# Optimization experiments

Measured on AMD Instinct MI355X. Metric: run time of the kernel, lower is better.

The kernel has to match this reference:

```python
import jax, jax.numpy as jnp
import numpy as np

H = 1024      # hidden_size
L = 4         # num_layers
DI = 2 * H    # d_inner (expand=2)
N = 16        # d_state
K = 4         # d_conv
BATCH = 2
S = 1024
EPS = 1e-5


def _layernorm(x, g, b):
    mu = jnp.mean(x, axis=-1, keepdims=True)
    xc = x - mu
    var = jnp.mean(xc * xc, axis=-1, keepdims=True)
    return xc * jax.lax.rsqrt(var + EPS) * g + b


def _causal_dwconv(x, w, b):
    # x: [B,S,DI], w: [DI,K], b: [DI]. Torch Conv1d(pad=K-1, groups=DI) truncated to S == causal left-pad conv.
    xp = jnp.pad(x, ((0, 0), (K - 1, 0), (0, 0)))
    s = x.shape[1]
    y = sum(xp[:, k:k + s, :] * w[:, k] for k in range(K))
    return y + b


def _forward(hidden_states, in_norm_g, in_norm_b, ln_g, ln_b, in_proj_w,
             conv_w, conv_b, x_proj_w, dt_proj_w, dt_proj_b, D,
             mamba_ln_g, mamba_ln_b, out_proj_w, op1_w, op1_b, op2_w, op2_b):
    dtype = hidden_states.dtype
    A = -jnp.arange(1, N + 1, dtype=dtype)  # [N]; == -exp(log(arange)), identical across d_inner rows
    x = _layernorm(hidden_states, in_norm_g, in_norm_b)
    for l in range(L):
        res_x = x
        xn = _layernorm(x, ln_g[l], ln_b[l])
        xr = jnp.einsum('bsh,ph->bsp', xn, in_proj_w[l])           # [B,S,2*DI]
        x_inner, res = jnp.split(xr, 2, axis=-1)
        x_inner = jax.nn.silu(x_inner)
        for c in range(2):
            x_inner = jax.nn.silu(_causal_dwconv(x_inner, conv_w[l, c], conv_b[l, c]))
        proj = jnp.einsum('bsd,pd->bsp', x_inner, x_proj_w[l])     # [B,S,1+2N]
        dt_raw, Bm, Cm = proj[..., :1], proj[..., 1:1 + N], proj[..., 1 + N:]
        dt = jax.nn.softplus(dt_raw * dt_proj_w[l][:, 0] + dt_proj_b[l])  # [B,S,DI]

        def step(h, inp_t):
            dt_t, x_t, B_t, C_t = inp_t                      # [B,DI],[B,DI],[B,N],[B,N]
            h = h + dt_t[..., None] * (h * A + x_t[..., None] * B_t[:, None, :])
            y = jnp.einsum('bdn,bn->bd', h, C_t)
            return h, y

        h0 = jnp.zeros((x.shape[0], DI, N), dtype=dtype)
        xs = (dt.transpose(1, 0, 2), x_inner.transpose(1, 0, 2),
              Bm.transpose(1, 0, 2), Cm.transpose(1, 0, 2))
        _, ys = jax.lax.scan(step, h0, xs)                   # ys: [S,B,DI]
        y = ys.transpose(1, 0, 2)
        y = y + x_inner * D[l]
        y = _layernorm(y, mamba_ln_g[l], mamba_ln_b[l])
        y = y * jax.nn.sigmoid(res)
        x = res_x + jnp.einsum('bsd,hd->bsh', y, out_proj_w[l])
    out = jax.nn.gelu(x @ op1_w.T + op1_b, approximate=False) @ op2_w.T + op2_b
    return out + hidden_states


def setup_inputs() -> dict:
    key = jax.random.key(0)
    ks = jax.random.split(key, 10)
    rn = lambda k, shape, s: jax.random.normal(k, shape, dtype=jnp.float32) * s
    return {
        'hidden_states': rn(ks[0], (BATCH, S, H), 1.0),
        'in_norm_g': jnp.ones((H,), jnp.float32),
        'in_norm_b': jnp.zeros((H,), jnp.float32),
        'ln_g': jnp.ones((L, H), jnp.float32),
        'ln_b': jnp.zeros((L, H), jnp.float32),
        'in_proj_w': rn(ks[1], (L, 2 * DI, H), 0.02),
        'conv_w': rn(ks[2], (L, 2, DI, K), 0.2),
        'conv_b': jnp.zeros((L, 2, DI), jnp.float32),
        'x_proj_w': rn(ks[3], (L, 1 + 2 * N, DI), 0.02),
        'dt_proj_w': rn(ks[4], (L, DI, 1), 0.01),
        'dt_proj_b': jnp.full((L, DI), -4.0, jnp.float32),  # keeps dt small -> stable scan
        'D': jnp.ones((L, DI), jnp.float32),
        'mamba_ln_g': jnp.ones((L, DI), jnp.float32),
        'mamba_ln_b': jnp.zeros((L, DI), jnp.float32),
        'out_proj_w': rn(ks[5], (L, H, DI), 0.02),
        'op1_w': rn(ks[6], (H, H), 0.02),
        'op1_b': jnp.zeros((H,), jnp.float32),
        'op2_w': rn(ks[7], (H, H), 0.02),
        'op2_b': jnp.zeros((H,), jnp.float32),
    }


def reference(hidden_states, in_norm_g, in_norm_b, ln_g, ln_b, in_proj_w,
              conv_w, conv_b, x_proj_w, dt_proj_w, dt_proj_b, D,
              mamba_ln_g, mamba_ln_b, out_proj_w, op1_w, op1_b, op2_w, op2_b):
    return _forward(hidden_states, in_norm_g, in_norm_b, ln_g, ln_b, in_proj_w,
                    conv_w, conv_b, x_proj_w, dt_proj_w, dt_proj_b, D,
                    mamba_ln_g, mamba_ln_b, out_proj_w, op1_w, op1_b, op2_w, op2_b)
```

## Files before the change

kernel.cpp:

```cpp
#include <hip/hip_runtime.h>
#include <hip/hip_bf16.h>
#include <math.h>

constexpr int HDIM = 1024;
constexpr int LNUM = 4;
constexpr int DINNER = 2048;
constexpr int KCONV = 4;
constexpr int NB = 2;
constexpr int SLEN = 1024;
constexpr int TOK = NB * SLEN;
constexpr float LNEPS = 1e-5f;

constexpr int NCHUNK = 32;
constexpr int CLEN = SLEN / NCHUNK;
constexpr int PROW = 36;
constexpr int XPN = 48;
constexpr int XSPLIT = 8;

typedef __attribute__((ext_vector_type(8))) short short8;
typedef __attribute__((ext_vector_type(4))) float f32x4;

__device__ __forceinline__ float bf2f(__hip_bfloat16 x) { return __bfloat162float(x); }
__device__ __forceinline__ __hip_bfloat16 f2bf(float x) { return __float2bfloat16(x); }
__device__ __forceinline__ float sigmoidf_(float x) { return 1.f / (1.f + __expf(-x)); }
__device__ __forceinline__ float siluf_(float x) { return x / (1.f + __expf(-x)); }
__device__ __forceinline__ float softplusf_(float x) { return (x > 20.f) ? x : log1pf(__expf(x)); }

__device__ __forceinline__ float ldin(const void* p, size_t i, int f) {
    return f ? ((const float*)p)[i] : bf2f(((const __hip_bfloat16*)p)[i]);
}

__device__ __forceinline__ void cp16(const void* g, void* l) {
    __builtin_amdgcn_global_load_lds(
        (const __attribute__((address_space(1))) unsigned int*)g,
        (__attribute__((address_space(3))) unsigned int*)l, 16, 0, 0);
}

__global__ void probe_k(const unsigned* __restrict__ dtb, int* __restrict__ flag)
{
    if (threadIdx.x == 0 && blockIdx.x == 0)
        *flag = (dtb[0] == 0xC0800000u) ? 1 : 0;
}

__global__ __launch_bounds__(256) void cvt_k(const void* __restrict__ in, size_t off,
                                             __hip_bfloat16* __restrict__ out, int n,
                                             const int* __restrict__ dflag)
{
    const int f = *dflag;
    int i = blockIdx.x * 256 + threadIdx.x;
    if (i < n) out[i] = f2bf(ldin(in, off + (size_t)i, f));
}

template<int MODE, int D>
__global__ __launch_bounds__(256) void ln_k(
    const void* __restrict__ in, const void* __restrict__ g, const void* __restrict__ b,
    size_t goff,
    float* __restrict__ outF, __hip_bfloat16* __restrict__ outB,
    const float* __restrict__ gate, int gstride, const int* __restrict__ dflag)
{
    const int f = *dflag;
    constexpr int EPT = D / 256;
    const int t = blockIdx.x, tid = threadIdx.x;
    float v[EPT];
    float s1 = 0.f, s2 = 0.f;
#pragma unroll
    for (int i = 0; i < EPT; ++i) {
        int idx = tid + i * 256;
        float val = (MODE == 0) ? ldin(in, (size_t)t * D + idx, f)
                                : ((const float*)in)[(size_t)t * D + idx];
        v[i] = val; s1 += val; s2 += val * val;
    }
#pragma unroll
    for (int off = 32; off; off >>= 1) { s1 += __shfl_down(s1, off); s2 += __shfl_down(s2, off); }
    __shared__ float rs[4], rq[4];
    const int w = tid >> 6, lane = tid & 63;
    if (lane == 0) { rs[w] = s1; rq[w] = s2; }
    __syncthreads();
    const float mu = (rs[0] + rs[1] + rs[2] + rs[3]) * (1.f / D);
    const float ms = (rq[0] + rq[1] + rq[2] + rq[3]) * (1.f / D);
    const float var = ms - mu * mu;
    const float rstd = rsqrtf((var > 0.f ? var : 0.f) + LNEPS);
#pragma unroll
    for (int i = 0; i < EPT; ++i) {
        int idx = tid + i * 256;
        float o = (v[i] - mu) * rstd * ldin(g, goff + idx, f) + ldin(b, goff + idx, f);
        if (MODE == 2) o *= sigmoidf_(gate[(size_t)t * gstride + idx]);
        if (MODE == 0) outF[(size_t)t * D + idx] = o;
        else           outB[(size_t)t * D + idx] = f2bf(o);
    }
}

template<int EPI>
__global__ __launch_bounds__(256) void gemm_bt(
    const unsigned short* __restrict__ A, const unsigned short* __restrict__ B,
    int M, int N, int Kd,
    float* __restrict__ Cf, __hip_bfloat16* __restrict__ Cb,
    const float* __restrict__ resF, const void* __restrict__ bias,
    const void* __restrict__ resB, void* __restrict__ outD,
    const int* __restrict__ dflag)
{
    const int f = (EPI >= 2) ? *dflag : 0;
    __shared__ __align__(16) unsigned short As[2][128 * 32];
    __shared__ __align__(16) unsigned short Bs[2][128 * 32];
    const int tid = threadIdx.x;
    const int m0 = blockIdx.x * 128, n0 = blockIdx.y * 128;
    const int klen = Kd / (int)gridDim.z;
    const int kstart = (int)blockIdx.z * klen;
    const int nK = klen >> 5;
    const int wave = tid >> 6, lane = tid & 63;
    const int wm = (wave & 1) * 64, wn = (wave >> 1) * 64;
    const int quad = lane >> 4, l16 = lane & 15;
    f32x4 acc[4][4];
#pragma unroll
    for (int i = 0; i < 4; ++i)
#pragma unroll
        for (int j = 0; j < 4; ++j) acc[i][j] = (f32x4){0.f, 0.f, 0.f, 0.f};

    const int r1 = tid >> 2, kc1 = (tid & 3) * 8;
    const int r2 = r1 + 64;

    {
        const int k0 = kstart;
        cp16(&A[(size_t)(m0 + r1) * Kd + k0 + kc1], &As[0][tid * 8]);
        cp16(&A[(size_t)(m0 + r2) * Kd + k0 + kc1], &As[0][(tid + 256) * 8]);
        cp16(&B[(size_t)(n0 + r1) * Kd + k0 + kc1], &Bs[0][tid * 8]);
        cp16(&B[(size_t)(n0 + r2) * Kd + k0 + kc1], &Bs[0][(tid + 256) * 8]);
    }
    for (int kk = 0; kk < nK; ++kk) {
        __syncthreads();
        if (kk + 1 < nK) {
            const int k0 = kstart + ((kk + 1) << 5);
            const int nb = (kk + 1) & 1;
            cp16(&A[(size_t)(m0 + r1) * Kd + k0 + kc1], &As[nb][tid * 8]);
            cp16(&A[(size_t)(m0 + r2) * Kd + k0 + kc1], &As[nb][(tid + 256) * 8]);
            cp16(&B[(size_t)(n0 + r1) * Kd + k0 + kc1], &Bs[nb][tid * 8]);
            cp16(&B[(size_t)(n0 + r2) * Kd + k0 + kc1], &Bs[nb][(tid + 256) * 8]);
        }
        const int cb = kk & 1;
        short8 af[4], bfm[4];
#pragma unroll
        for (int i = 0; i < 4; ++i) af[i]  = *(const short8*)&As[cb][(wm + i * 16 + l16) * 32 + quad * 8];
#pragma unroll
        for (int j = 0; j < 4; ++j) bfm[j] = *(const short8*)&Bs[cb][(wn + j * 16 + l16) * 32 + quad * 8];
#pragma unroll
        for (int i = 0; i < 4; ++i)
#pragma unroll
            for (int j = 0; j < 4; ++j)
                acc[i][j] = __builtin_amdgcn_mfma_f32_16x16x32_bf16(af[i], bfm[j], acc[i][j], 0, 0, 0);
    }

#pragma unroll
    for (int i = 0; i < 4; ++i)
#pragma unroll
        for (int j = 0; j < 4; ++j)
#pragma unroll
            for (int r = 0; r < 4; ++r) {
                const int row = m0 + wm + i * 16 + quad * 4 + r;
                const int col = n0 + wn + j * 16 + l16;
                const size_t off = (size_t)row * N + col;
                float vv = acc[i][j][r];
                if (EPI == 0) {
                    Cf[off] = vv;
                } else if (EPI == 1) {
                    Cf[off] = vv + resF[off];
                } else if (EPI == 2) {
                    float z = vv + ldin(bias, col, f);
                    Cb[off] = f2bf(0.5f * z * (1.f + erff(z * 0.70710678118f)));
                } else if (EPI == 3) {
                    float z = vv + ldin(bias, col, f) + ldin(resB, off, f);
                    if (f) ((float*)outD)[off] = z;
                    else   ((__hip_bfloat16*)outD)[off] = f2bf(z);
                } else {
                    atomicAdd(&Cf[off], vv);
                }
            }
}

__global__ __launch_bounds__(256) void conv2_fused(
    const float* __restrict__ xin, int in_stride,
    const void* __restrict__ cw, const void* __restrict__ cb, int layer,
    float* __restrict__ out, __hip_bfloat16* __restrict__ outb,
    const int* __restrict__ dflag)
{
    const int f = *dflag;
    const int d = blockIdx.x * 256 + threadIdx.x;
    const int s0 = blockIdx.y * 64;
    const int b = blockIdx.z;
    float w1k[4], w2k[4];
#pragma unroll
    for (int k = 0; k < 4; ++k) {
        w1k[k] = ldin(cw, (((size_t)layer * 2 + 0) * DINNER + d) * KCONV + k, f);
        w2k[k] = ldin(cw, (((size_t)layer * 2 + 1) * DINNER + d) * KCONV + k, f);
    }
    const float b1 = ldin(cb, ((size_t)layer * 2 + 0) * DINNER + d, f);
    const float b2 = ldin(cb, ((size_t)layer * 2 + 1) * DINNER + d, f);
    const float* base = xin + (size_t)b * SLEN * in_stride + d;
    const size_t obase = (size_t)b * SLEN * DINNER + d;
    float r1 = 0.f, r2 = 0.f, r3 = 0.f;
    float c1a = 0.f, c1b = 0.f, c1c = 0.f;
    for (int s = s0 - 6; s < s0 + 64; ++s) {
        float xs = 0.f;
        if (s >= 0) xs = siluf_(base[(size_t)s * in_stride]);
        float c1 = 0.f;
        if (s >= 0) {
            float t = fmaf(w1k[0], r3, fmaf(w1k[1], r2, fmaf(w1k[2], r1, fmaf(w1k[3], xs, b1))));
            c1 = siluf_(t);
        }
        if (s >= s0) {
            float t2 = fmaf(w2k[0], c1c, fmaf(w2k[1], c1b, fmaf(w2k[2], c1a, fmaf(w2k[3], c1, b2))));
            float v = siluf_(t2);
            out[obase + (size_t)s * DINNER] = v;
            outb[obase + (size_t)s * DINNER] = f2bf(v);
        }
        r3 = r2; r2 = r1; r1 = xs;
        c1c = c1b; c1b = c1a; c1a = c1;
    }
}

__global__ __launch_bounds__(256) void xproj_mfma(
    const unsigned short* __restrict__ A, const unsigned short* __restrict__ B,
    float* __restrict__ proj)
{
    __shared__ __align__(16) unsigned short As[2][128 * 32];
    __shared__ __align__(16) unsigned short Bs[2][XPN * 32];
    const int tid = threadIdx.x;
    const int m0 = blockIdx.x * 128;
    const int k0base = blockIdx.y * (DINNER / XSPLIT);
    constexpr int nK = (DINNER / XSPLIT) >> 5;
    const int wave = tid >> 6, lane = tid & 63;
    const int wm = wave * 32;
    const int quad = lane >> 4, l16 = lane & 15;
    f32x4 acc[2][3];
#pragma unroll
    for (int i = 0; i < 2; ++i)
#pragma unroll
        for (int j = 0; j < 3; ++j) acc[i][j] = (f32x4){0.f, 0.f, 0.f, 0.f};

    const int r1 = tid >> 2, kc1 = (tid & 3) * 8;
    {
        const int k0 = k0base;
        cp16(&A[(size_t)(m0 + r1) * DINNER + k0 + kc1], &As[0][tid * 8]);
        cp16(&A[(size_t)(m0 + r1 + 64) * DINNER + k0 + kc1], &As[0][(tid + 256) * 8]);
        if (tid < XPN * 4)
            cp16(&B[(size_t)r1 * DINNER + k0 + kc1], &Bs[0][tid * 8]);
    }
    for (int kk = 0; kk < nK; ++kk) {
        __syncthreads();
        if (kk + 1 < nK) {
            const int k0 = k0base + ((kk + 1) << 5);
            const int nb = (kk + 1) & 1;
            cp16(&A[(size_t)(m0 + r1) * DINNER + k0 + kc1], &As[nb][tid * 8]);
            cp16(&A[(size_t)(m0 + r1 + 64) * DINNER + k0 + kc1], &As[nb][(tid + 256) * 8]);
            if (tid < XPN * 4)
                cp16(&B[(size_t)r1 * DINNER + k0 + kc1], &Bs[nb][tid * 8]);
        }
        const int cb = kk & 1;
        short8 af[2], bfm[3];
#pragma unroll
        for (int i = 0; i < 2; ++i) af[i]  = *(const short8*)&As[cb][(wm + i * 16 + l16) * 32 + quad * 8];
#pragma unroll
        for (int j = 0; j < 3; ++j) bfm[j] = *(const short8*)&Bs[cb][(j * 16 + l16) * 32 + quad * 8];
#pragma unroll
        for (int i = 0; i < 2; ++i)
#pragma unroll
            for (int j = 0; j < 3; ++j)
                acc[i][j] = __builtin_amdgcn_mfma_f32_16x16x32_bf16(af[i], bfm[j], acc[i][j], 0, 0, 0);
    }
#pragma unroll
    for (int i = 0; i < 2; ++i)
#pragma unroll
        for (int j = 0; j < 3; ++j) {
            const int col = j * 16 + l16;
            if (col < 33) {
#pragma unroll
                for (int r = 0; r < 4; ++r) {
                    const int row = m0 + wm + i * 16 + quad * 4 + r;
                    atomicAdd(&proj[(size_t)row * 33 + col], acc[i][j][r]);
                }
            }
        }
}

__device__ __forceinline__ void load_proj_chunk(float* sp, const float* __restrict__ proj,
                                                int b, int c, int tid)
{
    const float* psrc = proj + ((size_t)b * SLEN + (size_t)c * CLEN) * 33;
    for (int i = tid; i < CLEN * 33; i += 256) {
        int s = i / 33, p = i - s * 33;
        sp[s * PROW + (p == 0 ? 32 : p - 1)] = psrc[i];
    }
}

__global__ __launch_bounds__(256) void scan_partA(
    const float* __restrict__ proj, const float* __restrict__ xin,
    const void* __restrict__ dtw, const void* __restrict__ dtb, int layer,
    float* __restrict__ hloc, float* __restrict__ cumA_g,
    const int* __restrict__ dflag)
{
    const int f = *dflag;
    __shared__ __align__(16) float sp[CLEN * PROW];
    const int tid = threadIdx.x;
    const int d = blockIdx.x * 256 + tid;
    const int c = blockIdx.y, b = blockIdx.z;
    load_proj_chunk(sp, proj, b, c, tid);
    const float w_ = ldin(dtw, (size_t)layer * DINNER + d, f);
    const float bb = ldin(dtb, (size_t)layer * DINNER + d, f);
    __syncthreads();
    float h[16], ca[16];
#pragma unroll
    for (int n = 0; n < 16; ++n) { h[n] = 0.f; ca[n] = 1.f; }
    const float* xrow = xin + ((size_t)b * SLEN + (size_t)c * CLEN) * DINNER + d;
    float xt_next = xrow[0];
    for (int s = 0; s < CLEN; ++s) {
        const float xt = xt_next;
        if (s + 1 < CLEN) xt_next = xrow[(size_t)(s + 1) * DINNER];
        const float* row = &sp[s * PROW];
        const float dt = softplusf_(fmaf(row[32], w_, bb));
        const float u = dt * xt;
#pragma unroll
        for (int n = 0; n < 16; ++n) {
            const float a = fmaf(dt, -(float)(n + 1), 1.f);
            h[n] = fmaf(h[n], a, u * row[n]);
            ca[n] *= a;
        }
    }
    const size_t base = (((size_t)b * NCHUNK + c) * 16) * DINNER + d;
#pragma unroll
    for (int n = 0; n < 16; ++n) {
        hloc[base + (size_t)n * DINNER] = h[n];
        cumA_g[base + (size_t)n * DINNER] = ca[n];
    }
}

__global__ __launch_bounds__(256) void scan_combine(
    const float* __restrict__ hloc, const float* __restrict__ cumA_g,
    float* __restrict__ hin)
{
    const int idx = blockIdx.x * 256 + threadIdx.x;
    const int d = idx & (DINNER - 1);
    const int n = (idx >> 11) & 15;
    const int b = idx >> 15;
    float h = 0.f;
    for (int c = 0; c < NCHUNK; ++c) {
        const size_t off = (((size_t)b * NCHUNK + c) * 16 + n) * DINNER + d;
        hin[off] = h;
        h = fmaf(cumA_g[off], h, hloc[off]);
    }
}

__global__ __launch_bounds__(256) void scan_partC(
    const float* __restrict__ proj, const float* __restrict__ xin,
    const void* __restrict__ dtw, const void* __restrict__ dtb,
    const void* __restrict__ Dp, int layer,
    const float* __restrict__ hin, float* __restrict__ y,
    const int* __restrict__ dflag)
{
    const int f = *dflag;
    __shared__ __align__(16) float sp[CLEN * PROW];
    const int tid = threadIdx.x;
    const int d = blockIdx.x * 256 + tid;
    const int c = blockIdx.y, b = blockIdx.z;
    load_proj_chunk(sp, proj, b, c, tid);
    const float w_ = ldin(dtw, (size_t)layer * DINNER + d, f);
    const float bb = ldin(dtb, (size_t)layer * DINNER + d, f);
    const float Dd = ldin(Dp,  (size_t)layer * DINNER + d, f);
    __syncthreads();
    float h[16];
    const size_t base = (((size_t)b * NCHUNK + c) * 16) * DINNER + d;
#pragma unroll
    for (int n = 0; n < 16; ++n) h[n] = hin[base + (size_t)n * DINNER];
    const float* xrow = xin + ((size_t)b * SLEN + (size_t)c * CLEN) * DINNER + d;
    float* yrow = y + ((size_t)b * SLEN + (size_t)c * CLEN) * DINNER + d;
    float xt_next = xrow[0];
    for (int s = 0; s < CLEN; ++s) {
        const float xt = xt_next;
        if (s + 1 < CLEN) xt_next = xrow[(size_t)(s + 1) * DINNER];
        const float* row = &sp[s * PROW];
        const float dt = softplusf_(fmaf(row[32], w_, bb));
        const float u = dt * xt;
        float yp = 0.f;
#pragma unroll
        for (int n = 0; n < 16; ++n) {
            const float a = fmaf(dt, -(float)(n + 1), 1.f);
            h[n] = fmaf(h[n], a, u * row[n]);
            yp = fmaf(h[n], row[16 + n], yp);
        }
        yrow[(size_t)s * DINNER] = yp + xt * Dd;
    }
}

__global__ __launch_bounds__(256) void cast_f2b(const float* __restrict__ in,
                                                __hip_bfloat16* __restrict__ out, int n)
{
    int i = blockIdx.x * 256 + threadIdx.x;
    if (i < n) out[i] = f2bf(in[i]);
}

extern "C" void kernel_launch(void* const* d_in, const int* in_sizes, int n_in,
                              void* d_out, int out_size, void* d_ws, size_t ws_size,
                              hipStream_t stream)
{
    (void)in_sizes; (void)n_in; (void)out_size;
    char* p = (char*)d_ws;
    int* flag = (int*)p; p += 256;
    float* x   = (float*)p; p += (size_t)TOK * HDIM * 4;
    float* xr  = (float*)p; p += (size_t)TOK * 2 * DINNER * 4;
    float* c2  = (float*)p; p += (size_t)TOK * DINNER * 4;
    float* yb  = (float*)p; p += (size_t)TOK * DINNER * 4;
    float* proj= (float*)p; p += ((size_t)TOK * 33 * 4 + 255) & ~(size_t)255;
    float* hin = (float*)p; p += (size_t)NB * NCHUNK * 16 * DINNER * 4;
    __hip_bfloat16* xn  = (__hip_bfloat16*)p; p += (size_t)TOK * HDIM * 2;
    __hip_bfloat16* y2  = (__hip_bfloat16*)p; p += (size_t)TOK * DINNER * 2;
    __hip_bfloat16* c2b = (__hip_bfloat16*)p; p += (size_t)TOK * DINNER * 2;
    __hip_bfloat16* wx  = (__hip_bfloat16*)p; p += (size_t)LNUM * XPN * DINNER * 2;
    __hip_bfloat16* t1 = (__hip_bfloat16*)xr;
    float* hloc = yb;
    float* cumA = yb + (size_t)NB * NCHUNK * 16 * DINNER;

    const size_t IPL = (size_t)2 * DINNER * HDIM;
    const size_t OPL = (size_t)HDIM * DINNER;
    const size_t MLPW = (size_t)HDIM * HDIM;

    size_t used = (size_t)(p - (char*)d_ws);
    const bool bulk = (used + (IPL * LNUM + OPL * LNUM + 2 * MLPW) * 2) <= ws_size;

    __hip_bfloat16 *wi[LNUM], *wo[LNUM], *w1, *w2;
    if (bulk) {
        for (int l = 0; l < LNUM; ++l) { wi[l] = (__hip_bfloat16*)p; p += IPL * 2; }
        for (int l = 0; l < LNUM; ++l) { wo[l] = (__hip_bfloat16*)p; p += OPL * 2; }
        w1 = (__hip_bfloat16*)p; p += MLPW * 2;
        w2 = (__hip_bfloat16*)p; p += MLPW * 2;
    } else {
        __hip_bfloat16* slotA = (__hip_bfloat16*)p; p += IPL * 2;
        __hip_bfloat16* slotB = (__hip_bfloat16*)p; p += OPL * 2;
        for (int l = 0; l < LNUM; ++l) { wi[l] = slotA; wo[l] = slotB; }
        w1 = slotA; w2 = slotB;
    }

    probe_k<<<1, 64, 0, stream>>>((const unsigned*)d_in[10], flag);

    hipMemsetAsync(wx, 0, (size_t)LNUM * XPN * DINNER * 2, stream);
    for (int l = 0; l < LNUM; ++l)
        cvt_k<<<(33 * DINNER + 255) / 256, 256, 0, stream>>>(
            d_in[8], (size_t)l * 33 * DINNER, wx + (size_t)l * XPN * DINNER, 33 * DINNER, flag);

    if (bulk) {
        cvt_k<<<(int)((IPL * LNUM + 255) / 256), 256, 0, stream>>>(d_in[5], 0, wi[0], (int)(IPL * LNUM), flag);
        cvt_k<<<(int)((OPL * LNUM + 255) / 256), 256, 0, stream>>>(d_in[14], 0, wo[0], (int)(OPL * LNUM), flag);
        cvt_k<<<(int)((MLPW + 255) / 256), 256, 0, stream>>>(d_in[15], 0, w1, (int)MLPW, flag);
        cvt_k<<<(int)((MLPW + 255) / 256), 256, 0, stream>>>(d_in[17], 0, w2, (int)MLPW, flag);
    }

    ln_k<0, HDIM><<<TOK, 256, 0, stream>>>(d_in[0], d_in[1], d_in[2], 0, x, nullptr, nullptr, 0, flag);

    for (int l = 0; l < LNUM; ++l) {
        ln_k<1, HDIM><<<TOK, 256, 0, stream>>>(x, d_in[3], d_in[4], (size_t)l * HDIM,
                                               nullptr, xn, nullptr, 0, flag);
        if (!bulk)
            cvt_k<<<(int)((IPL + 255) / 256), 256, 0, stream>>>(d_in[5], (size_t)l * IPL, wi[l], (int)IPL, flag);
        gemm_bt<0><<<dim3(TOK / 128, (2 * DINNER) / 128), 256, 0, stream>>>(
            (const unsigned short*)xn, (const unsigned short*)wi[l],
            TOK, 2 * DINNER, HDIM, xr, nullptr, nullptr, nullptr, nullptr, nullptr, flag);

        conv2_fused<<<dim3(DINNER / 256, SLEN / 64, NB), 256, 0, stream>>>(
            xr, 2 * DINNER, d_in[6], d_in[7], l, c2, c2b, flag);

        hipMemsetAsync(proj, 0, (size_t)TOK * 33 * 4, stream);
        xproj_mfma<<<dim3(TOK / 128, XSPLIT), 256, 0, stream>>>(
            (const unsigned short*)c2b, (const unsigned short*)(wx + (size_t)l * XPN * DINNER), proj);

        scan_partA<<<dim3(DINNER / 256, NCHUNK, NB), 256, 0, stream>>>(
            proj, c2, d_in[9], d_in[10], l, hloc, cumA, flag);
        scan_combine<<<(NB * 16 * DINNER) / 256, 256, 0, stream>>>(hloc, cumA, hin);
        scan_partC<<<dim3(DINNER / 256, NCHUNK, NB), 256, 0, stream>>>(
            proj, c2, d_in[9], d_in[10], d_in[11], l, hin, yb, flag);

        ln_k<2, DINNER><<<TOK, 256, 0, stream>>>(yb, d_in[12], d_in[13], (size_t)l * DINNER,
                                                 nullptr, y2, xr + DINNER, 2 * DINNER, flag);

        if (!bulk)
            cvt_k<<<(int)((OPL + 255) / 256), 256, 0, stream>>>(d_in[14], (size_t)l * OPL, wo[l], (int)OPL, flag);
        gemm_bt<4><<<dim3(TOK / 128, HDIM / 128, 2), 256, 0, stream>>>(
            (const unsigned short*)y2, (const unsigned short*)wo[l],
            TOK, HDIM, DINNER, x, nullptr, nullptr, nullptr, nullptr, nullptr, flag);
    }

    cast_f2b<<<(TOK * HDIM + 255) / 256, 256, 0, stream>>>(x, xn, TOK * HDIM);
    if (!bulk) {
        cvt_k<<<(int)((MLPW + 255) / 256), 256, 0, stream>>>(d_in[15], 0, w1, (int)MLPW, flag);
        cvt_k<<<(int)((MLPW + 255) / 256), 256, 0, stream>>>(d_in[17], 0, w2, (int)MLPW, flag);
    }
    gemm_bt<2><<<dim3(TOK / 128, HDIM / 128), 256, 0, stream>>>(
        (const unsigned short*)xn, (const unsigned short*)w1,
        TOK, HDIM, HDIM, nullptr, t1, nullptr, d_in[16], nullptr, nullptr, flag);
    gemm_bt<3><<<dim3(TOK / 128, HDIM / 128), 256, 0, stream>>>(
        (const unsigned short*)t1, (const unsigned short*)w2,
        TOK, HDIM, HDIM, nullptr, nullptr, nullptr, d_in[18], d_in[0], d_out, flag);
}
```

Measured before the change: 1.026 ms.

## Drop dtype probe, vectorize elementwise kernels, replace atomics with split-K partial buffers

Removes the runtime bf16/fp32 dtype probe and assumes fp32 inputs throughout. Element-wise conversion, layernorm and cast kernels now use float4 loads and stores. The atomicAdd accumulation in the x-projection and out-projection GEMMs is replaced by writing per-split partial buffers, which separate combine kernels then sum. This trades atomic traffic for extra launches and an extra read and write pass over the partials.

Result: faster. 936.1 us (-8.7%).

```diff
diff --git a/kernel.cpp b/kernel.cpp
--- a/kernel.cpp
+++ b/kernel.cpp
@@ -20,15 +20,14 @@
 typedef __attribute__((ext_vector_type(8))) short short8;
 typedef __attribute__((ext_vector_type(4))) float f32x4;
 
-__device__ __forceinline__ float bf2f(__hip_bfloat16 x) { return __bfloat162float(x); }
 __device__ __forceinline__ __hip_bfloat16 f2bf(float x) { return __float2bfloat16(x); }
+__device__ __forceinline__ unsigned short f2bfu(float x) {
+    __hip_bfloat16 h = __float2bfloat16(x);
+    return *(unsigned short*)&h;
+}
 __device__ __forceinline__ float sigmoidf_(float x) { return 1.f / (1.f + __expf(-x)); }
 __device__ __forceinline__ float siluf_(float x) { return x / (1.f + __expf(-x)); }
 __device__ __forceinline__ float softplusf_(float x) { return (x > 20.f) ? x : log1pf(__expf(x)); }
-
-__device__ __forceinline__ float ldin(const void* p, size_t i, int f) {
-    return f ? ((const float*)p)[i] : bf2f(((const __hip_bfloat16*)p)[i]);
-}
 
 __device__ __forceinline__ void cp16(const void* g, void* l) {
     __builtin_amdgcn_global_load_lds(
@@ -36,39 +35,54 @@
         (__attribute__((address_space(3))) unsigned int*)l, 16, 0, 0);
 }
 
-__global__ void probe_k(const unsigned* __restrict__ dtb, int* __restrict__ flag)
-{
-    if (threadIdx.x == 0 && blockIdx.x == 0)
-        *flag = (dtb[0] == 0xC0800000u) ? 1 : 0;
-}
-
-__global__ __launch_bounds__(256) void cvt_k(const void* __restrict__ in, size_t off,
-                                             __hip_bfloat16* __restrict__ out, int n,
-                                             const int* __restrict__ dflag)
-{
-    const int f = *dflag;
-    int i = blockIdx.x * 256 + threadIdx.x;
-    if (i < n) out[i] = f2bf(ldin(in, off + (size_t)i, f));
+__global__ __launch_bounds__(256) void cvt_k(const float* __restrict__ in,
+                                             __hip_bfloat16* __restrict__ out, int n4)
+{
+    const int i = blockIdx.x * 256 + threadIdx.x;
+    if (i >= n4) return;
+    float4 v = ((const float4*)in)[i];
+    ushort4 o;
+    o.x = f2bfu(v.x); o.y = f2bfu(v.y); o.z = f2bfu(v.z); o.w = f2bfu(v.w);
+    ((ushort4*)out)[i] = o;
+}
+
+__global__ __launch_bounds__(256) void cvtwx_k(const float* __restrict__ in,
+                                               __hip_bfloat16* __restrict__ out)
+{
+    const int i = blockIdx.x * 256 + threadIdx.x;
+    if (i >= LNUM * XPN * DINNER / 4) return;
+    const int e = i * 4;
+    const int l = e / (XPN * DINNER);
+    const int rem = e - l * XPN * DINNER;
+    const int r = rem >> 11;
+    const int col = rem & (DINNER - 1);
+    ushort4 o;
+    if (r < 33) {
+        float4 v = *(const float4*)&in[(((size_t)l * 33 + r) << 11) + col];
+        o.x = f2bfu(v.x); o.y = f2bfu(v.y); o.z = f2bfu(v.z); o.w = f2bfu(v.w);
+    } else {
+        o.x = o.y = o.z = o.w = 0;
+    }
+    ((ushort4*)out)[i] = o;
 }
 
 template<int MODE, int D>
 __global__ __launch_bounds__(256) void ln_k(
-    const void* __restrict__ in, const void* __restrict__ g, const void* __restrict__ b,
-    size_t goff,
+    const float* __restrict__ in, const float* __restrict__ g, const float* __restrict__ b,
     float* __restrict__ outF, __hip_bfloat16* __restrict__ outB,
-    const float* __restrict__ gate, int gstride, const int* __restrict__ dflag)
-{
-    const int f = *dflag;
-    constexpr int EPT = D / 256;
+    const float* __restrict__ gate, int gstride)
+{
+    constexpr int EPT = D / 1024;
     const int t = blockIdx.x, tid = threadIdx.x;
-    float v[EPT];
+    float4 v[EPT];
     float s1 = 0.f, s2 = 0.f;
 #pragma unroll
     for (int i = 0; i < EPT; ++i) {
-        int idx = tid + i * 256;
-        float val = (MODE == 0) ? ldin(in, (size_t)t * D + idx, f)
-                                : ((const float*)in)[(size_t)t * D + idx];
-        v[i] = val; s1 += val; s2 += val * val;
+        const int idx = (tid + i * 256) * 4;
+        float4 val = *(const float4*)&in[(size_t)t * D + idx];
+        v[i] = val;
+        s1 += val.x + val.y + val.z + val.w;
+        s2 += val.x * val.x + val.y * val.y + val.z * val.z + val.w * val.w;
     }
 #pragma unroll
     for (int off = 32; off; off >>= 1) { s1 += __shfl_down(s1, off); s2 += __shfl_down(s2, off); }
@@ -82,11 +96,26 @@
     const float rstd = rsqrtf((var > 0.f ? var : 0.f) + LNEPS);
 #pragma unroll
     for (int i = 0; i < EPT; ++i) {
-        int idx = tid + i * 256;
-        float o = (v[i] - mu) * rstd * ldin(g, goff + idx, f) + ldin(b, goff + idx, f);
-        if (MODE == 2) o *= sigmoidf_(gate[(size_t)t * gstride + idx]);
-        if (MODE == 0) outF[(size_t)t * D + idx] = o;
-        else           outB[(size_t)t * D + idx] = f2bf(o);
+        const int idx = (tid + i * 256) * 4;
+        const float4 gg = *(const float4*)&g[idx];
+        const float4 bb = *(const float4*)&b[idx];
+        float4 o;
+        o.x = (v[i].x - mu) * rstd * gg.x + bb.x;
+        o.y = (v[i].y - mu) * rstd * gg.y + bb.y;
+        o.z = (v[i].z - mu) * rstd * gg.z + bb.z;
+        o.w = (v[i].w - mu) * rstd * gg.w + bb.w;
+        if (MODE == 2) {
+            const float4 gt = *(const float4*)&gate[(size_t)t * gstride + idx];
+            o.x *= sigmoidf_(gt.x); o.y *= sigmoidf_(gt.y);
+            o.z *= sigmoidf_(gt.z); o.w *= sigmoidf_(gt.w);
+        }
+        if (MODE == 0) {
+            ((float4*)outF)[((size_t)t * D + idx) >> 2] = o;
+        } else {
+            ushort4 u;
+            u.x = f2bfu(o.x); u.y = f2bfu(o.y); u.z = f2bfu(o.z); u.w = f2bfu(o.w);
+            ((ushort4*)outB)[((size_t)t * D + idx) >> 2] = u;
+        }
     }
 }
 
@@ -95,11 +124,9 @@
     const unsigned short* __restrict__ A, const unsigned short* __restrict__ B,
     int M, int N, int Kd,
     float* __restrict__ Cf, __hip_bfloat16* __restrict__ Cb,
-    const float* __restrict__ resF, const void* __restrict__ bias,
-    const void* __restrict__ resB, void* __restrict__ outD,
-    const int* __restrict__ dflag)
-{
-    const int f = (EPI >= 2) ? *dflag : 0;
+    const float* __restrict__ bias, const float* __restrict__ res,
+    float* __restrict__ Of)
+{
     __shared__ __align__(16) unsigned short As[2][128 * 32];
     __shared__ __align__(16) unsigned short Bs[2][128 * 32];
     const int tid = threadIdx.x;
@@ -149,6 +176,7 @@
                 acc[i][j] = __builtin_amdgcn_mfma_f32_16x16x32_bf16(af[i], bfm[j], acc[i][j], 0, 0, 0);
     }
 
+    const size_t zoff = (EPI == 1) ? (size_t)blockIdx.z * M * N : 0;
 #pragma unroll
     for (int i = 0; i < 4; ++i)
 #pragma unroll
@@ -162,38 +190,57 @@
                 if (EPI == 0) {
                     Cf[off] = vv;
                 } else if (EPI == 1) {
-                    Cf[off] = vv + resF[off];
+                    Cf[zoff + off] = vv;
                 } else if (EPI == 2) {
-                    float z = vv + ldin(bias, col, f);
+                    float z = vv + bias[col];
                     Cb[off] = f2bf(0.5f * z * (1.f + erff(z * 0.70710678118f)));
-                } else if (EPI == 3) {
-                    float z = vv + ldin(bias, col, f) + ldin(resB, off, f);
-                    if (f) ((float*)outD)[off] = z;
-                    else   ((__hip_bfloat16*)outD)[off] = f2bf(z);
                 } else {
-                    atomicAdd(&Cf[off], vv);
+                    Of[off] = vv + bias[col] + res[off];
                 }
             }
 }
 
+__global__ __launch_bounds__(256) void xcomb_k(const float* __restrict__ part,
+                                               float* __restrict__ x, int n4)
+{
+    const int i = blockIdx.x * 256 + threadIdx.x;
+    if (i >= n4) return;
+    float4 a = ((const float4*)part)[i];
+    float4 b = ((const float4*)part)[i + n4];
+    float4 v = ((const float4*)x)[i];
+    v.x += a.x + b.x; v.y += a.y + b.y; v.z += a.z + b.z; v.w += a.w + b.w;
+    ((float4*)x)[i] = v;
+}
+
+__global__ __launch_bounds__(256) void pcomb_k(const float* __restrict__ ppart,
+                                               float* __restrict__ proj)
+{
+    const int idx = blockIdx.x * 256 + threadIdx.x;
+    if (idx >= TOK * 33) return;
+    const int t = idx / 33, p2 = idx - t * 33;
+    float s = 0.f;
+#pragma unroll
+    for (int k = 0; k < XSPLIT; ++k)
+        s += ppart[(size_t)k * TOK * XPN + (size_t)t * XPN + p2];
+    proj[idx] = s;
+}
+
 __global__ __launch_bounds__(256) void conv2_fused(
     const float* __restrict__ xin, int in_stride,
-    const void* __restrict__ cw, const void* __restrict__ cb, int layer,
-    float* __restrict__ out, __hip_bfloat16* __restrict__ outb,
-    const int* __restrict__ dflag)
-{
-    const int f = *dflag;
+    const float* __restrict__ cw, const float* __restrict__ cb, int layer,
+    float* __restrict__ out, __hip_bfloat16* __restrict__ outb)
+{
     const int d = blockIdx.x * 256 + threadIdx.x;
     const int s0 = blockIdx.y * 64;
     const int b = blockIdx.z;
     float w1k[4], w2k[4];
 #pragma unroll
     for (int k = 0; k < 4; ++k) {
-        w1k[k] = ldin(cw, (((size_t)layer * 2 + 0) * DINNER + d) * KCONV + k, f);
-        w2k[k] = ldin(cw, (((size_t)layer * 2 + 1) * DINNER + d) * KCONV + k, f);
-    }
-    const float b1 = ldin(cb, ((size_t)layer * 2 + 0) * DINNER + d, f);
-    const float b2 = ldin(cb, ((size_t)layer * 2 + 1) * DINNER + d, f);
+        w1k[k] = cw[(((size_t)layer * 2 + 0) * DINNER + d) * KCONV + k];
+        w2k[k] = cw[(((size_t)layer * 2 + 1) * DINNER + d) * KCONV + k];
+    }
+    const float b1 = cb[((size_t)layer * 2 + 0) * DINNER + d];
+    const float b2 = cb[((size_t)layer * 2 + 1) * DINNER + d];
     const float* base = xin + (size_t)b * SLEN * in_stride + d;
     const size_t obase = (size_t)b * SLEN * DINNER + d;
     float r1 = 0.f, r2 = 0.f, r3 = 0.f;
@@ -219,7 +266,7 @@
 
 __global__ __launch_bounds__(256) void xproj_mfma(
     const unsigned short* __restrict__ A, const unsigned short* __restrict__ B,
-    float* __restrict__ proj)
+    float* __restrict__ ppart)
 {
     __shared__ __align__(16) unsigned short As[2][128 * 32];
     __shared__ __align__(16) unsigned short Bs[2][XPN * 32];
@@ -266,17 +313,16 @@
             for (int j = 0; j < 3; ++j)
                 acc[i][j] = __builtin_amdgcn_mfma_f32_16x16x32_bf16(af[i], bfm[j], acc[i][j], 0, 0, 0);
     }
+    float* pp = ppart + (size_t)blockIdx.y * TOK * XPN;
 #pragma unroll
     for (int i = 0; i < 2; ++i)
 #pragma unroll
         for (int j = 0; j < 3; ++j) {
             const int col = j * 16 + l16;
-            if (col < 33) {
-#pragma unroll
-                for (int r = 0; r < 4; ++r) {
-                    const int row = m0 + wm + i * 16 + quad * 4 + r;
-                    atomicAdd(&proj[(size_t)row * 33 + col], acc[i][j][r]);
-                }
+#pragma unroll
+            for (int r = 0; r < 4; ++r) {
+                const int row = m0 + wm + i * 16 + quad * 4 + r;
+                pp[(size_t)row * XPN + col] = acc[i][j][r];
             }
         }
 }
@@ -293,18 +339,16 @@
 
 __global__ __launch_bounds__(256) void scan_partA(
     const float* __restrict__ proj, const float* __restrict__ xin,
-    const void* __restrict__ dtw, const void* __restrict__ dtb, int layer,
-    float* __restrict__ hloc, float* __restrict__ cumA_g,
-    const int* __restrict__ dflag)
-{
-    const int f = *dflag;
+    const float* __restrict__ dtw, const float* __restrict__ dtb, int layer,
+    float* __restrict__ hloc, float* __restrict__ cumA_g)
+{
     __shared__ __align__(16) float sp[CLEN * PROW];
     const int tid = threadIdx.x;
     const int d = blockIdx.x * 256 + tid;
     const int c = blockIdx.y, b = blockIdx.z;
     load_proj_chunk(sp, proj, b, c, tid);
-    const float w_ = ldin(dtw, (size_t)layer * DINNER + d, f);
-    const float bb = ldin(dtb, (size_t)layer * DINNER + d, f);
+    const float w_ = dtw[(size_t)layer * DINNER + d];
+    const float bb = dtb[(size_t)layer * DINNER + d];
     __syncthreads();
     float h[16], ca[16];
 #pragma unroll
@@ -350,20 +394,18 @@
 
 __global__ __launch_bounds__(256) void scan_partC(
     const float* __restrict__ proj, const float* __restrict__ xin,
-    const void* __restrict__ dtw, const void* __restrict__ dtb,
-    const void* __restrict__ Dp, int layer,
-    const float* __restrict__ hin, float* __restrict__ y,
-    const int* __restrict__ dflag)
-{
-    const int f = *dflag;
+    const float* __restrict__ dtw, const float* __restrict__ dtb,
+    const float* __restrict__ Dp, int layer,
+    const float* __restrict__ hin, float* __restrict__ y)
+{
     __shared__ __align__(16) float sp[CLEN * PROW];
     const int tid = threadIdx.x;
     const int d = blockIdx.x * 256 + tid;
     const int c = blockIdx.y, b = blockIdx.z;
     load_proj_chunk(sp, proj, b, c, tid);
-    const float w_ = ldin(dtw, (size_t)layer * DINNER + d, f);
-    const float bb = ldin(dtb, (size_t)layer * DINNER + d, f);
-    const float Dd = ldin(Dp,  (size_t)layer * DINNER + d, f);
+    const float w_ = dtw[(size_t)layer * DINNER + d];
+    const float bb = dtb[(size_t)layer * DINNER + d];
+    const float Dd = Dp[(size_t)layer * DINNER + d];
     __syncthreads();
     float h[16];
     const size_t base = (((size_t)b * NCHUNK + c) * 16) * DINNER + d;
@@ -390,10 +432,14 @@
 }
 
 __global__ __launch_bounds__(256) void cast_f2b(const float* __restrict__ in,
-                                                __hip_bfloat16* __restrict__ out, int n)
+                                                __hip_bfloat16* __restrict__ out, int n4)
 {
     int i = blockIdx.x * 256 + threadIdx.x;
-    if (i < n) out[i] = f2bf(in[i]);
+    if (i >= n4) return;
+    float4 v = ((const float4*)in)[i];
+    ushort4 u;
+    u.x = f2bfu(v.x); u.y = f2bfu(v.y); u.z = f2bfu(v.z); u.w = f2bfu(v.w);
+    ((ushort4*)out)[i] = u;
 }
 
 extern "C" void kernel_launch(void* const* d_in, const int* in_sizes, int n_in,
@@ -401,14 +447,34 @@
                               hipStream_t stream)
 {
     (void)in_sizes; (void)n_in; (void)out_size;
+    const float* hs   = (const float*)d_in[0];
+    const float* ing  = (const float*)d_in[1];
+    const float* inb  = (const float*)d_in[2];
+    const float* lng  = (const float*)d_in[3];
+    const float* lnb  = (const float*)d_in[4];
+    const float* ipw  = (const float*)d_in[5];
+    const float* cw   = (const float*)d_in[6];
+    const float* cbp  = (const float*)d_in[7];
+    const float* xpw  = (const float*)d_in[8];
+    const float* dtw  = (const float*)d_in[9];
+    const float* dtb  = (const float*)d_in[10];
+    const float* Dp   = (const float*)d_in[11];
+    const float* mlg  = (const float*)d_in[12];
+    const float* mlb  = (const float*)d_in[13];
+    const float* opw  = (const float*)d_in[14];
+    const float* w1f  = (const float*)d_in[15];
+    const float* b1f  = (const float*)d_in[16];
+    const float* w2f  = (const float*)d_in[17];
+    const float* b2f  = (const float*)d_in[18];
+
     char* p = (char*)d_ws;
-    int* flag = (int*)p; p += 256;
     float* x   = (float*)p; p += (size_t)TOK * HDIM * 4;
     float* xr  = (float*)p; p += (size_t)TOK * 2 * DINNER * 4;
     float* c2  = (float*)p; p += (size_t)TOK * DINNER * 4;
     float* yb  = (float*)p; p += (size_t)TOK * DINNER * 4;
     float* proj= (float*)p; p += ((size_t)TOK * 33 * 4 + 255) & ~(size_t)255;
     float* hin = (float*)p; p += (size_t)NB * NCHUNK * 16 * DINNER * 4;
+    float* ppart=(float*)p; p += (size_t)XSPLIT * TOK * XPN * 4;
     __hip_bfloat16* xn  = (__hip_bfloat16*)p; p += (size_t)TOK * HDIM * 2;
     __hip_bfloat16* y2  = (__hip_bfloat16*)p; p += (size_t)TOK * DINNER * 2;
     __hip_bfloat16* c2b = (__hip_bfloat16*)p; p += (size_t)TOK * DINNER * 2;
@@ -416,6 +482,7 @@
     __hip_bfloat16* t1 = (__hip_bfloat16*)xr;
     float* hloc = yb;
     float* cumA = yb + (size_t)NB * NCHUNK * 16 * DINNER;
+    float* opart = c2;
 
     const size_t IPL = (size_t)2 * DINNER * HDIM;
     const size_t OPL = (size_t)HDIM * DINNER;
@@ -437,63 +504,59 @@
         w1 = slotA; w2 = slotB;
     }
 
-    probe_k<<<1, 64, 0, stream>>>((const unsigned*)d_in[10], flag);
-
-    hipMemsetAsync(wx, 0, (size_t)LNUM * XPN * DINNER * 2, stream);
-    for (int l = 0; l < LNUM; ++l)
-        cvt_k<<<(33 * DINNER + 255) / 256, 256, 0, stream>>>(
-            d_in[8], (size_t)l * 33 * DINNER, wx + (size_t)l * XPN * DINNER, 33 * DINNER, flag);
+    cvtwx_k<<<(LNUM * XPN * DINNER / 4 + 255) / 256, 256, 0, stream>>>(xpw, wx);
 
     if (bulk) {
-        cvt_k<<<(int)((IPL * LNUM + 255) / 256), 256, 0, stream>>>(d_in[5], 0, wi[0], (int)(IPL * LNUM), flag);
-        cvt_k<<<(int)((OPL * LNUM + 255) / 256), 256, 0, stream>>>(d_in[14], 0, wo[0], (int)(OPL * LNUM), flag);
-        cvt_k<<<(int)((MLPW + 255) / 256), 256, 0, stream>>>(d_in[15], 0, w1, (int)MLPW, flag);
-        cvt_k<<<(int)((MLPW + 255) / 256), 256, 0, stream>>>(d_in[17], 0, w2, (int)MLPW, flag);
-    }
-
-    ln_k<0, HDIM><<<TOK, 256, 0, stream>>>(d_in[0], d_in[1], d_in[2], 0, x, nullptr, nullptr, 0, flag);
+        cvt_k<<<(int)(IPL * LNUM / 4 / 256), 256, 0, stream>>>(ipw, wi[0], (int)(IPL * LNUM / 4));
+        cvt_k<<<(int)(OPL * LNUM / 4 / 256), 256, 0, stream>>>(opw, wo[0], (int)(OPL * LNUM / 4));
+        cvt_k<<<(int)(MLPW / 4 / 256), 256, 0, stream>>>(w1f, w1, (int)(MLPW / 4));
+        cvt_k<<<(int)(MLPW / 4 / 256), 256, 0, stream>>>(w2f, w2, (int)(MLPW / 4));
+    }
+
+    ln_k<0, HDIM><<<TOK, 256, 0, stream>>>(hs, ing, inb, x, nullptr, nullptr, 0);
 
     for (int l = 0; l < LNUM; ++l) {
-        ln_k<1, HDIM><<<TOK, 256, 0, stream>>>(x, d_in[3], d_in[4], (size_t)l * HDIM,
-                                               nullptr, xn, nullptr, 0, flag);
+        ln_k<1, HDIM><<<TOK, 256, 0, stream>>>(x, lng + (size_t)l * HDIM, lnb + (size_t)l * HDIM,
+                                               nullptr, xn, nullptr, 0);
         if (!bulk)
-            cvt_k<<<(int)((IPL + 255) / 256), 256, 0, stream>>>(d_in[5], (size_t)l * IPL, wi[l], (int)IPL, flag);
+            cvt_k<<<(int)(IPL / 4 / 256), 256, 0, stream>>>(ipw + (size_t)l * IPL, wi[l], (int)(IPL / 4));
         gemm_bt<0><<<dim3(TOK / 128, (2 * DINNER) / 128), 256, 0, stream>>>(
             (const unsigned short*)xn, (const unsigned short*)wi[l],
-            TOK, 2 * DINNER, HDIM, xr, nullptr, nullptr, nullptr, nullptr, nullptr, flag);
+            TOK, 2 * DINNER, HDIM, xr, nullptr, nullptr, nullptr, nullptr);
 
         conv2_fused<<<dim3(DINNER / 256, SLEN / 64, NB), 256, 0, stream>>>(
-            xr, 2 * DINNER, d_in[6], d_in[7], l, c2, c2b, flag);
-
-        hipMemsetAsync(proj, 0, (size_t)TOK * 33 * 4, stream);
+            xr, 2 * DINNER, cw, cbp, l, c2, c2b);
+
         xproj_mfma<<<dim3(TOK / 128, XSPLIT), 256, 0, stream>>>(
-            (const unsigned short*)c2b, (const unsigned short*)(wx + (size_t)l * XPN * DINNER), proj);
+            (const unsigned short*)c2b, (const unsigned short*)(wx + (size_t)l * XPN * DINNER), ppart);
+        pcomb_k<<<(TOK * 33 + 255) / 256, 256, 0, stream>>>(ppart, proj);
 
         scan_partA<<<dim3(DINNER / 256, NCHUNK, NB), 256, 0, stream>>>(
-            proj, c2, d_in[9], d_in[10], l, hloc, cumA, flag);
+            proj, c2, dtw, dtb, l, hloc, cumA);
         scan_combine<<<(NB * 16 * DINNER) / 256, 256, 0, stream>>>(hloc, cumA, hin);
         scan_partC<<<dim3(DINNER / 256, NCHUNK, NB), 256, 0, stream>>>(
-            proj, c2, d_in[9], d_in[10], d_in[11], l, hin, yb, flag);
-
-        ln_k<2, DINNER><<<TOK, 256, 0, stream>>>(yb, d_in[12], d_in[13], (size_t)l * DINNER,
-                                                 nullptr, y2, xr + DINNER, 2 * DINNER, flag);
+            proj, c2, dtw, dtb, Dp, l, hin, yb);
+
+        ln_k<2, DINNER><<<TOK, 256, 0, stream>>>(yb, mlg + (size_t)l * DINNER, mlb + (size_t)l * DINNER,
+                                                 nullptr, y2, xr + DINNER, 2 * DINNER);
 
         if (!bulk)
-            cvt_k<<<(int)((OPL + 255) / 256), 256, 0, stream>>>(d_in[14], (size_t)l * OPL, wo[l], (int)OPL, flag);
-        gemm_bt<4><<<dim3(TOK / 128, HDIM / 128, 2), 256, 0, stream>>>(
+            cvt_k<<<(int)(OPL / 4 / 256), 256, 0, stream>>>(opw + (size_t)l * OPL, wo[l], (int)(OPL / 4));
+        gemm_bt<1><<<dim3(TOK / 128, HDIM / 128, 2), 256, 0, stream>>>(
             (const unsigned short*)y2, (const unsigned short*)wo[l],
-            TOK, HDIM, DINNER, x, nullptr, nullptr, nullptr, nullptr, nullptr, flag);
-    }
-
-    cast_f2b<<<(TOK * HDIM + 255) / 256, 256, 0, stream>>>(x, xn, TOK * HDIM);
+            TOK, HDIM, DINNER, opart, nullptr, nullptr, nullptr, nullptr);
+        xcomb_k<<<(TOK * HDIM / 4 + 255) / 256, 256, 0, stream>>>(opart, x, TOK * HDIM / 4);
+    }
+
+    cast_f2b<<<(TOK * HDIM / 4 + 255) / 256, 256, 0, stream>>>(x, xn, TOK * HDIM / 4);
     if (!bulk) {
-        cvt_k<<<(int)((MLPW + 255) / 256), 256, 0, stream>>>(d_in[15], 0, w1, (int)MLPW, flag);
-        cvt_k<<<(int)((MLPW + 255) / 256), 256, 0, stream>>>(d_in[17], 0, w2, (int)MLPW, flag);
+        cvt_k<<<(int)(MLPW / 4 / 256), 256, 0, stream>>>(w1f, w1, (int)(MLPW / 4));
+        cvt_k<<<(int)(MLPW / 4 / 256), 256, 0, stream>>>(w2f, w2, (int)(MLPW / 4));
     }
     gemm_bt<2><<<dim3(TOK / 128, HDIM / 128), 256, 0, stream>>>(
         (const unsigned short*)xn, (const unsigned short*)w1,
-        TOK, HDIM, HDIM, nullptr, t1, nullptr, d_in[16], nullptr, nullptr, flag);
+        TOK, HDIM, HDIM, nullptr, t1, b1f, nullptr, nullptr);
     gemm_bt<3><<<dim3(TOK / 128, HDIM / 128), 256, 0, stream>>>(
         (const unsigned short*)t1, (const unsigned short*)w2,
-        TOK, HDIM, HDIM, nullptr, nullptr, nullptr, d_in[18], d_in[0], d_out, flag);
-}
+        TOK, HDIM, HDIM, nullptr, nullptr, b2f, hs, (float*)d_out);
+}
```
